# Optimization experiments

Hardware: AMD Instinct MI355X
Metric: run time of the kernel (lower is better)

The kernel has to match this reference:

```python
import jax, jax.numpy as jnp
import numpy as np

KH = KW = 3
SH = SW = 1
PH = PW = 1


def _im2col(x, kh, kw, sh, sw, ph, pw):
    # x: [N, C, H, W] -> cols: [N, C*kh*kw, H_out*W_out], ordering (C, kh, kw)
    N, C, H, W = x.shape
    H_out = (H + 2 * ph - kh) // sh + 1
    W_out = (W + 2 * pw - kw) // sw + 1
    x_pad = jnp.pad(x, ((0, 0), (0, 0), (ph, ph), (pw, pw)))
    # fixed small loop over kernel offsets (kh*kw = 9), strided slices
    patches = [x_pad[:, :, i:i + sh * H_out:sh, j:j + sw * W_out:sw]
               for i in range(kh) for j in range(kw)]  # each [N, C, H_out, W_out]
    cols = jnp.stack(patches, axis=2)  # [N, C, kh*kw, H_out, W_out]
    cols = cols.reshape(N, C * kh * kw, H_out * W_out)
    return cols, H_out, W_out


def setup_inputs() -> dict:
    key = jax.random.key(0)
    k1, k2, k3 = jax.random.split(key, 3)
    x = jax.random.normal(k1, (16, 128, 56, 56), dtype=jnp.float32)
    weight = jax.random.normal(k2, (256, 128, 3, 3), dtype=jnp.float32) * 0.05
    fan_in = 128 * 3 * 3
    bound = 1.0 / fan_in ** 0.5
    bias = jax.random.uniform(k3, (256,), dtype=jnp.float32, minval=-bound, maxval=bound)
    return {"x": x, "weight": weight, "bias": bias}


def reference(x, weight, bias):
    # im2col unfold + (analog) matmul conv; noise_cfg=None -> plain matmul
    cols, H_out, W_out = _im2col(x, KH, KW, SH, SW, PH, PW)  # [N, K, L]
    N = cols.shape[0]
    Cout = weight.shape[0]
    Wmat = weight.reshape(Cout, -1)  # [Cout, K], K = C*kh*kw
    # y[n, l, o] = sum_k cols[n, k, l] * Wmat[o, k]  (AnalogMatMulFn without noise)
    y = jnp.einsum('nkl,ok->nol', cols, Wmat)  # [N, Cout, L]
    y = y.reshape(N, Cout, H_out, W_out)
    y = y + bias[None, :, None, None]
    return y
```

## Files before the change

kernel.cpp:

```cpp
#include <hip/hip_runtime.h>
#include <hip/hip_bf16.h>
#include <stdint.h>


typedef __attribute__((ext_vector_type(8))) short short8;
typedef __attribute__((ext_vector_type(4))) float floatx4;

__device__ static inline void gload_lds16(const void* g, void* l) {
  typedef const __attribute__((address_space(1))) unsigned int* gp_t;
  typedef __attribute__((address_space(3))) unsigned int* lp_t;
  __builtin_amdgcn_global_load_lds((gp_t)(uintptr_t)g, (lp_t)(uint32_t)(uintptr_t)l,
                                   16, 0, 0);
}

__global__ __launch_bounds__(256)
void pre_kernel(const float* __restrict__ x, const float* __restrict__ wsrc,
                __hip_bfloat16* __restrict__ xp, __hip_bfloat16* __restrict__ wt) {
  const int b = blockIdx.x;
  if (b < 16 * 58) {
    const int n = b / 58, hp = b % 58;
    __hip_bfloat16* dst = xp + (size_t)(n * 58 + hp) * 58 * 128;
    if (hp == 0 || hp == 57) {
      const uint4 z = {0, 0, 0, 0};
      uint4* p = (uint4*)dst;
      for (int i = threadIdx.x; i < 928; i += 256) p[i] = z;
      return;
    }
    const int h = hp - 1;
    __shared__ float tile[128][57];
    const float* src = x + (size_t)n * (128 * 3136) + h * 56;
    for (int i = threadIdx.x; i < 128 * 14; i += 256) {
      const int c = i / 14, q = i - c * 14;
      const float4 v = ((const float4*)(src + (size_t)c * 3136))[q];
      tile[c][4 * q + 0] = v.x;
      tile[c][4 * q + 1] = v.y;
      tile[c][4 * q + 2] = v.z;
      tile[c][4 * q + 3] = v.w;
    }
    __syncthreads();
    if (threadIdx.x < 32) {
      const uint4 z = {0, 0, 0, 0};
      const int col = (threadIdx.x >> 4) * 57;
      ((uint4*)(dst + (size_t)col * 128))[threadIdx.x & 15] = z;
    }
    __hip_bfloat16* di = dst + 128;
    for (int i = threadIdx.x; i < 56 * 16; i += 256) {
      const int w = i >> 4, c8 = (i & 15) * 8;
      union { uint4 u; __hip_bfloat16 hh[8]; } pk;
#pragma unroll
      for (int j = 0; j < 8; ++j) pk.hh[j] = __float2bfloat16(tile[c8 + j][w]);
      *(uint4*)(di + (size_t)w * 128 + c8) = pk.u;
    }
  } else {
    const int base = (b - 928) * 256 + threadIdx.x;
    for (int t = base; t < 256 * 9 * 128; t += 36 * 256) {
      const int e = t & 7;
      const int rr = (t >> 3) & 15;
      const int q = (t >> 7) & 3;
      const int ks = (t >> 9) & 1;
      const int ch = (t >> 10) & 1;
      const int t11 = t >> 11;
      const int kq = t11 % 9;
      const int g = t11 / 9;
      const int cout = g * 16 + rr;
      const int c = ch * 64 + ks * 32 + q * 8 + e;
      wt[t] = __float2bfloat16(wsrc[(size_t)(cout * 128 + c) * 9 + kq]);
    }
  }
}

__global__ __launch_bounds__(256, 3)
void conv_gemm_kernel(const __hip_bfloat16* __restrict__ xp,
                      const __hip_bfloat16* __restrict__ wt,
                      const float* __restrict__ bias,
                      float* __restrict__ out) {
  __shared__ __align__(16) char smem[49152];

  const int tid = threadIdx.x;
  const int lane = tid & 63;
  const int wave = tid >> 6;
  const int col = lane & 15;
  const int quad = lane >> 4;

  const int id = blockIdx.x;
  const int xcd = id & 7;
  const int r = id >> 3;
  const int mt_ = r / 98;
  const int nt_ = xcd * 98 + (r - mt_ * 98);
  const int m0 = mt_ * 128;
  const int n0 = nt_ * 64;

  const int nimg0 = n0 / 3136;
  const int rem0 = n0 - nimg0 * 3136;
  const int hh0 = rem0 / 56;
  const int ww0 = rem0 - hh0 * 56;
  const int P0 = (nimg0 * 58 + hh0) * 58 + ww0;
  const char* pbase = (const char*)xp + (size_t)P0 * 256;

#pragma unroll
  for (int i = 0; i < 12; ++i) {
    const int j = i * 256 + tid;
    const int row = j >> 4;
    const int slot = j & 15;
    gload_lds16(pbase + row * 256 + ((slot ^ (row & 7)) << 4),
                smem + i * 4096 + wave * 1024);
  }

  const char* wtb = (const char*)wt;
  const int gbase = (m0 >> 4) + wave * 2;
  const char* pA0 = wtb + (size_t)gbase * 36864 + lane * 16;
  const char* pA1 = pA0 + 36864;

  short8 areg[3][2][2];
#pragma unroll
  for (int s0 = 0; s0 < 2; ++s0) {
    const int ofs = (s0 & 1) * 2048;
#pragma unroll
    for (int ks = 0; ks < 2; ++ks) {
      areg[s0][0][ks] = *(const short8*)(pA0 + ofs + ks * 1024);
      areg[s0][1][ks] = *(const short8*)(pA1 + ofs + ks * 1024);
    }
  }

  int rbase[4];
#pragma unroll
  for (int nt = 0; nt < 4; ++nt) {
    const int pix = n0 + nt * 16 + col;
    const int ni = pix / 3136;
    const int re = pix - ni * 3136;
    const int ph = re / 56;
    const int pw = re - ph * 56;
    rbase[nt] = (ni * 58 + ph) * 58 + pw - P0;
  }

  floatx4 acc[2][4];
#pragma unroll
  for (int a = 0; a < 2; ++a)
#pragma unroll
    for (int c = 0; c < 4; ++c) acc[a][c] = (floatx4)0.f;

  __syncthreads();

  short8 bfr[2][4][2];
#pragma unroll
  for (int nt = 0; nt < 4; ++nt) {
    const int rowB = rbase[nt];
#pragma unroll
    for (int ks = 0; ks < 2; ++ks) {
      const int cB = ks * 4 + quad;
      const int pos = cB ^ (rowB & 7);
      bfr[0][nt][ks] = *(const short8*)(smem + rowB * 256 + (pos << 4));
    }
  }

#pragma unroll
  for (int s = 0; s < 18; ++s) {
    if (s < 16) {
      const int s2 = s + 2;
      const int ofs = (s2 >> 1) * 4096 + (s2 & 1) * 2048;
      const int slot = s2 % 3;
#pragma unroll
      for (int ks = 0; ks < 2; ++ks) {
        areg[slot][0][ks] = *(const short8*)(pA0 + ofs + ks * 1024);
        areg[slot][1][ks] = *(const short8*)(pA1 + ofs + ks * 1024);
      }
    }
    if (s < 17) {
      const int s1 = s + 1;
      const int kq1 = s1 >> 1, ch1 = s1 & 1;
      const int kh1 = kq1 / 3;
      const int tofs1 = kh1 * 58 + (kq1 - kh1 * 3);
      const int nb = s1 & 1;
#pragma unroll
      for (int nt = 0; nt < 4; ++nt) {
        const int rowB = rbase[nt] + tofs1;
#pragma unroll
        for (int ks = 0; ks < 2; ++ks) {
          const int cB = ch1 * 8 + ks * 4 + quad;
          const int pos = cB ^ (rowB & 7);
          bfr[nb][nt][ks] = *(const short8*)(smem + rowB * 256 + (pos << 4));
        }
      }
    }
    const int ca = s % 3, cb = s & 1;
#pragma unroll
    for (int ks = 0; ks < 2; ++ks)
#pragma unroll
      for (int mt = 0; mt < 2; ++mt)
#pragma unroll
        for (int nt = 0; nt < 4; ++nt)
          acc[mt][nt] = __builtin_amdgcn_mfma_f32_16x16x32_bf16(
              areg[ca][mt][ks], bfr[cb][nt][ks], acc[mt][nt], 0, 0, 0);
  }

  const int rb = quad * 4;
#pragma unroll
  for (int nt = 0; nt < 4; ++nt) {
    const int pix = n0 + nt * 16 + col;
    const int nimg = pix / 3136;
    const int rem = pix - nimg * 3136;
    float* op = out + (size_t)nimg * (256 * 3136) + rem;
#pragma unroll
    for (int mt = 0; mt < 2; ++mt) {
      const int mb = m0 + wave * 32 + mt * 16 + rb;
#pragma unroll
      for (int rr = 0; rr < 4; ++rr) {
        op[(size_t)(mb + rr) * 3136] = acc[mt][nt][rr] + bias[mb + rr];
      }
    }
  }
}

__global__ __launch_bounds__(256)
void direct_conv_kernel(const float* __restrict__ x, const float* __restrict__ wgt,
                        const float* __restrict__ bias, float* __restrict__ out) {
  const long t = (long)blockIdx.x * 256 + threadIdx.x;
  if (t >= 16L * 256 * 3136) return;
  const int w = t % 56;
  const int h = (t / 56) % 56;
  const int o = (t / 3136) % 256;
  const int n = t / (256L * 3136);
  float s = bias[o];
  for (int c = 0; c < 128; ++c)
    for (int kh = 0; kh < 3; ++kh) {
      const int hh = h + kh - 1;
      if (hh < 0 || hh >= 56) continue;
      for (int kw = 0; kw < 3; ++kw) {
        const int ww = w + kw - 1;
        if (ww < 0 || ww >= 56) continue;
        s += x[((size_t)(n * 128 + c) * 56 + hh) * 56 + ww] *
             wgt[((size_t)(o * 128 + c) * 3 + kh) * 3 + kw];
      }
    }
  out[t] = s;
}

extern "C" void kernel_launch(void* const* d_in, const int* in_sizes, int n_in,
                              void* d_out, int out_size, void* d_ws, size_t ws_size,
                              hipStream_t stream) {
  const float* x = (const float*)d_in[0];
  const float* w = (const float*)d_in[1];
  const float* b = (const float*)d_in[2];
  float* out = (float*)d_out;

  const size_t xp_bytes = (size_t)16 * 58 * 58 * 128 * 2;
  const size_t wt_bytes = (size_t)256 * 9 * 128 * 2;

  if (ws_size >= xp_bytes + wt_bytes) {
    __hip_bfloat16* xp = (__hip_bfloat16*)d_ws;
    __hip_bfloat16* wt = (__hip_bfloat16*)((char*)d_ws + xp_bytes);
    hipLaunchKernelGGL(pre_kernel, dim3(16 * 58 + 36), dim3(256), 0, stream,
                       x, w, xp, wt);
    hipLaunchKernelGGL(conv_gemm_kernel, dim3(1568), dim3(256), 0, stream,
                       xp, wt, b, out);
  } else {
    const long total = 16L * 256 * 3136;
    hipLaunchKernelGGL(direct_conv_kernel, dim3((unsigned)((total + 255) / 256)),
                       dim3(256), 0, stream, x, w, b, out);
  }
}
```

Baseline: 126.7 us.

## Cover all 256 output channels per block, halving grid and reusing input tile

Each block now computes all 256 output channels for its 64-pixel tile, where before it computed 128. Each wave handles 64 channels with a 4x4 MFMA accumulator grid, and the grid drops from 1568 to 784 blocks. The K loop is restructured to 36 steps with double-buffered A registers and one k-slice per step. This removes the duplicated loading of the input halo tile into LDS across two M-tiles and raises MFMA work per LDS read. The cost is more accumulator registers, fewer blocks for the 256 CUs, and less A prefetch depth.

Result: slower. 141.2 us (+11.4%).

```diff
diff --git a/kernel.cpp b/kernel.cpp
--- a/kernel.cpp
+++ b/kernel.cpp
@@ -84,10 +84,7 @@
 
   const int id = blockIdx.x;
   const int xcd = id & 7;
-  const int r = id >> 3;
-  const int mt_ = r / 98;
-  const int nt_ = xcd * 98 + (r - mt_ * 98);
-  const int m0 = mt_ * 128;
+  const int nt_ = xcd * 98 + (id >> 3);
   const int n0 = nt_ * 64;
 
   const int nimg0 = n0 / 3136;
@@ -107,20 +104,14 @@
   }
 
   const char* wtb = (const char*)wt;
-  const int gbase = (m0 >> 4) + wave * 2;
-  const char* pA0 = wtb + (size_t)gbase * 36864 + lane * 16;
-  const char* pA1 = pA0 + 36864;
-
-  short8 areg[3][2][2];
-#pragma unroll
-  for (int s0 = 0; s0 < 2; ++s0) {
-    const int ofs = (s0 & 1) * 2048;
-#pragma unroll
-    for (int ks = 0; ks < 2; ++ks) {
-      areg[s0][0][ks] = *(const short8*)(pA0 + ofs + ks * 1024);
-      areg[s0][1][ks] = *(const short8*)(pA1 + ofs + ks * 1024);
-    }
-  }
+  const char* pA[4];
+#pragma unroll
+  for (int mt = 0; mt < 4; ++mt)
+    pA[mt] = wtb + (size_t)(wave * 4 + mt) * 36864 + lane * 16;
+
+  short8 areg[2][4];
+#pragma unroll
+  for (int mt = 0; mt < 4; ++mt) areg[0][mt] = *(const short8*)(pA[mt]);
 
   int rbase[4];
 #pragma unroll
@@ -133,64 +124,50 @@
     rbase[nt] = (ni * 58 + ph) * 58 + pw - P0;
   }
 
-  floatx4 acc[2][4];
-#pragma unroll
-  for (int a = 0; a < 2; ++a)
+  floatx4 acc[4][4];
+#pragma unroll
+  for (int a = 0; a < 4; ++a)
 #pragma unroll
     for (int c = 0; c < 4; ++c) acc[a][c] = (floatx4)0.f;
 
   __syncthreads();
 
-  short8 bfr[2][4][2];
+  short8 bfr[2][4];
 #pragma unroll
   for (int nt = 0; nt < 4; ++nt) {
     const int rowB = rbase[nt];
-#pragma unroll
-    for (int ks = 0; ks < 2; ++ks) {
-      const int cB = ks * 4 + quad;
-      const int pos = cB ^ (rowB & 7);
-      bfr[0][nt][ks] = *(const short8*)(smem + rowB * 256 + (pos << 4));
-    }
-  }
-
-#pragma unroll
-  for (int s = 0; s < 18; ++s) {
-    if (s < 16) {
-      const int s2 = s + 2;
-      const int ofs = (s2 >> 1) * 4096 + (s2 & 1) * 2048;
-      const int slot = s2 % 3;
-#pragma unroll
-      for (int ks = 0; ks < 2; ++ks) {
-        areg[slot][0][ks] = *(const short8*)(pA0 + ofs + ks * 1024);
-        areg[slot][1][ks] = *(const short8*)(pA1 + ofs + ks * 1024);
-      }
-    }
-    if (s < 17) {
+    const int pos = quad ^ (rowB & 7);
+    bfr[0][nt] = *(const short8*)(smem + rowB * 256 + (pos << 4));
+  }
+
+#pragma unroll
+  for (int s = 0; s < 36; ++s) {
+    if (s < 35) {
       const int s1 = s + 1;
-      const int kq1 = s1 >> 1, ch1 = s1 & 1;
+      const int kq1 = s1 >> 2;
+      const int ksl = s1 & 3;
+      const int nb = s1 & 1;
+      const int ofs = kq1 * 4096 + ksl * 1024;
+#pragma unroll
+      for (int mt = 0; mt < 4; ++mt)
+        areg[nb][mt] = *(const short8*)(pA[mt] + ofs);
       const int kh1 = kq1 / 3;
       const int tofs1 = kh1 * 58 + (kq1 - kh1 * 3);
-      const int nb = s1 & 1;
 #pragma unroll
       for (int nt = 0; nt < 4; ++nt) {
         const int rowB = rbase[nt] + tofs1;
-#pragma unroll
-        for (int ks = 0; ks < 2; ++ks) {
-          const int cB = ch1 * 8 + ks * 4 + quad;
-          const int pos = cB ^ (rowB & 7);
-          bfr[nb][nt][ks] = *(const short8*)(smem + rowB * 256 + (pos << 4));
-        }
+        const int cB = ksl * 4 + quad;
+        const int pos = cB ^ (rowB & 7);
+        bfr[nb][nt] = *(const short8*)(smem + rowB * 256 + (pos << 4));
       }
     }
-    const int ca = s % 3, cb = s & 1;
-#pragma unroll
-    for (int ks = 0; ks < 2; ++ks)
-#pragma unroll
-      for (int mt = 0; mt < 2; ++mt)
-#pragma unroll
-        for (int nt = 0; nt < 4; ++nt)
-          acc[mt][nt] = __builtin_amdgcn_mfma_f32_16x16x32_bf16(
-              areg[ca][mt][ks], bfr[cb][nt][ks], acc[mt][nt], 0, 0, 0);
+    const int cb = s & 1;
+#pragma unroll
+    for (int mt = 0; mt < 4; ++mt)
+#pragma unroll
+      for (int nt = 0; nt < 4; ++nt)
+        acc[mt][nt] = __builtin_amdgcn_mfma_f32_16x16x32_bf16(
+            areg[cb][mt], bfr[cb][nt], acc[mt][nt], 0, 0, 0);
   }
 
   const int rb = quad * 4;
@@ -201,8 +178,8 @@
     const int rem = pix - nimg * 3136;
     float* op = out + (size_t)nimg * (256 * 3136) + rem;
 #pragma unroll
-    for (int mt = 0; mt < 2; ++mt) {
-      const int mb = m0 + wave * 32 + mt * 16 + rb;
+    for (int mt = 0; mt < 4; ++mt) {
+      const int mb = wave * 64 + mt * 16 + rb;
 #pragma unroll
       for (int rr = 0; rr < 4; ++rr) {
         op[(size_t)(mb + rr) * 3136] = acc[mt][nt][rr] + bias[mb + rr];
@@ -251,7 +228,7 @@
     __hip_bfloat16* wt = (__hip_bfloat16*)((char*)d_ws + xp_bytes);
     hipLaunchKernelGGL(pre_kernel, dim3(16 * 58 + 36), dim3(256), 0, stream,
                        x, w, xp, wt);
-    hipLaunchKernelGGL(conv_gemm_kernel, dim3(1568), dim3(256), 0, stream,
+    hipLaunchKernelGGL(conv_gemm_kernel, dim3(784), dim3(256), 0, stream,
                        xp, wt, b, out);
   } else {
     const long total = 16L * 256 * 3136;
```

## Shrink LDS tile and register buffers to raise occupancy, read third tap row from global

Applied to the files above, without the earlier changes.

Cuts the staged input tile in LDS from 48KB to 32KB, so the third kernel row (kh=2) is read straight from global/L2 instead of LDS. The A-fragment ring buffer drops from three stages to two, and the B fragments are split into two half-buffers loaded between the two k-sub-step MFMA groups. The launch bound goes from 3 to 4 blocks per SM. The aim is higher occupancy and fewer registers. The cost is uncoalesced, latency-exposed global loads for one third of the K steps and a shallower prefetch depth.

Result: slower. 148.5 us (+17.2%).

```diff
diff --git a/kernel.cpp b/kernel.cpp
--- a/kernel.cpp
+++ b/kernel.cpp
@@ -69,12 +69,12 @@
   }
 }
 
-__global__ __launch_bounds__(256, 3)
+__global__ __launch_bounds__(256, 4)
 void conv_gemm_kernel(const __hip_bfloat16* __restrict__ xp,
                       const __hip_bfloat16* __restrict__ wt,
                       const float* __restrict__ bias,
                       float* __restrict__ out) {
-  __shared__ __align__(16) char smem[49152];
+  __shared__ __align__(16) char smem[32768];
 
   const int tid = threadIdx.x;
   const int lane = tid & 63;
@@ -98,7 +98,7 @@
   const char* pbase = (const char*)xp + (size_t)P0 * 256;
 
 #pragma unroll
-  for (int i = 0; i < 12; ++i) {
+  for (int i = 0; i < 8; ++i) {
     const int j = i * 256 + tid;
     const int row = j >> 4;
     const int slot = j & 15;
@@ -111,15 +111,11 @@
   const char* pA0 = wtb + (size_t)gbase * 36864 + lane * 16;
   const char* pA1 = pA0 + 36864;
 
-  short8 areg[3][2][2];
-#pragma unroll
-  for (int s0 = 0; s0 < 2; ++s0) {
-    const int ofs = (s0 & 1) * 2048;
-#pragma unroll
-    for (int ks = 0; ks < 2; ++ks) {
-      areg[s0][0][ks] = *(const short8*)(pA0 + ofs + ks * 1024);
-      areg[s0][1][ks] = *(const short8*)(pA1 + ofs + ks * 1024);
-    }
+  short8 areg[2][2][2];
+#pragma unroll
+  for (int ks = 0; ks < 2; ++ks) {
+    areg[0][0][ks] = *(const short8*)(pA0 + ks * 1024);
+    areg[0][1][ks] = *(const short8*)(pA1 + ks * 1024);
   }
 
   int rbase[4];
@@ -141,56 +137,74 @@
 
   __syncthreads();
 
-  short8 bfr[2][4][2];
+  short8 bfrP[4], bfrQ[4];
 #pragma unroll
   for (int nt = 0; nt < 4; ++nt) {
     const int rowB = rbase[nt];
-#pragma unroll
-    for (int ks = 0; ks < 2; ++ks) {
-      const int cB = ks * 4 + quad;
-      const int pos = cB ^ (rowB & 7);
-      bfr[0][nt][ks] = *(const short8*)(smem + rowB * 256 + (pos << 4));
-    }
+    const int pos = quad ^ (rowB & 7);
+    bfrP[nt] = *(const short8*)(smem + rowB * 256 + (pos << 4));
   }
 
 #pragma unroll
   for (int s = 0; s < 18; ++s) {
-    if (s < 16) {
-      const int s2 = s + 2;
-      const int ofs = (s2 >> 1) * 4096 + (s2 & 1) * 2048;
-      const int slot = s2 % 3;
-#pragma unroll
-      for (int ks = 0; ks < 2; ++ks) {
-        areg[slot][0][ks] = *(const short8*)(pA0 + ofs + ks * 1024);
-        areg[slot][1][ks] = *(const short8*)(pA1 + ofs + ks * 1024);
-      }
-    }
+    const int kq = s >> 1, ch = s & 1;
+    const int kh = kq / 3;
+    const int tofs = kh * 58 + (kq - kh * 3);
+    const int ca = s & 1;
+
+    if (s < 17) {
+      const int s1 = s + 1;
+      const int ofs = (s1 >> 1) * 4096 + (s1 & 1) * 2048;
+      const int nb = s1 & 1;
+      areg[nb][0][0] = *(const short8*)(pA0 + ofs);
+      areg[nb][0][1] = *(const short8*)(pA0 + ofs + 1024);
+      areg[nb][1][0] = *(const short8*)(pA1 + ofs);
+      areg[nb][1][1] = *(const short8*)(pA1 + ofs + 1024);
+    }
+
+#pragma unroll
+    for (int nt = 0; nt < 4; ++nt) {
+      const int rowB = rbase[nt] + tofs;
+      const int cB = ch * 8 + 4 + quad;
+      if (kh < 2) {
+        const int pos = cB ^ (rowB & 7);
+        bfrQ[nt] = *(const short8*)(smem + rowB * 256 + (pos << 4));
+      } else {
+        bfrQ[nt] = *(const short8*)(pbase + rowB * 256 + (cB << 4));
+      }
+    }
+
+#pragma unroll
+    for (int mt = 0; mt < 2; ++mt)
+#pragma unroll
+      for (int nt = 0; nt < 4; ++nt)
+        acc[mt][nt] = __builtin_amdgcn_mfma_f32_16x16x32_bf16(
+            areg[ca][mt][0], bfrP[nt], acc[mt][nt], 0, 0, 0);
+
     if (s < 17) {
       const int s1 = s + 1;
       const int kq1 = s1 >> 1, ch1 = s1 & 1;
       const int kh1 = kq1 / 3;
       const int tofs1 = kh1 * 58 + (kq1 - kh1 * 3);
-      const int nb = s1 & 1;
 #pragma unroll
       for (int nt = 0; nt < 4; ++nt) {
         const int rowB = rbase[nt] + tofs1;
-#pragma unroll
-        for (int ks = 0; ks < 2; ++ks) {
-          const int cB = ch1 * 8 + ks * 4 + quad;
+        const int cB = ch1 * 8 + quad;
+        if (kh1 < 2) {
           const int pos = cB ^ (rowB & 7);
-          bfr[nb][nt][ks] = *(const short8*)(smem + rowB * 256 + (pos << 4));
+          bfrP[nt] = *(const short8*)(smem + rowB * 256 + (pos << 4));
+        } else {
+          bfrP[nt] = *(const short8*)(pbase + rowB * 256 + (cB << 4));
         }
       }
     }
-    const int ca = s % 3, cb = s & 1;
-#pragma unroll
-    for (int ks = 0; ks < 2; ++ks)
-#pragma unroll
-      for (int mt = 0; mt < 2; ++mt)
-#pragma unroll
-        for (int nt = 0; nt < 4; ++nt)
-          acc[mt][nt] = __builtin_amdgcn_mfma_f32_16x16x32_bf16(
-              areg[ca][mt][ks], bfr[cb][nt][ks], acc[mt][nt], 0, 0, 0);
+
+#pragma unroll
+    for (int mt = 0; mt < 2; ++mt)
+#pragma unroll
+      for (int nt = 0; nt < 4; ++nt)
+        acc[mt][nt] = __builtin_amdgcn_mfma_f32_16x16x32_bf16(
+            areg[ca][mt][1], bfrQ[nt], acc[mt][nt], 0, 0, 0);
   }
 
   const int rb = quad * 4;
```
